# Kernel optimization log

Measured on AMD Instinct MI355X. Metric: run time of the kernel, lower is better.

The kernel has to match this reference:

```python
import jax, jax.numpy as jnp
import numpy as np

B, C, H, W = 4, 256, 64, 64
G, K, PAD, STRIDE, DIL, DWK = 8, 3, 1, 1, 1, 3
P = K * K
GC = C // G


def _dwconv(x, w, b, pad):
    # x: (B,C,H,W), w: (C,1,k,k) depthwise
    y = jax.lax.conv_general_dilated(x, w, (1, 1), [(pad, pad), (pad, pad)],
                                     feature_group_count=C,
                                     dimension_numbers=('NCHW', 'OIHW', 'NCHW'))
    return y + b[None, :, None, None]


def _conv1x1(x, w, b):
    # x: (B,Cin,H,W), w: (Cin,Cout)
    return jnp.einsum('bchw,cd->bdhw', x, w) + b[None, :, None, None]


def _ln(x, g, b, eps=1e-5):
    mu = x.mean(-1, keepdims=True)
    var = ((x - mu) ** 2).mean(-1, keepdims=True)
    return (x - mu) * jax.lax.rsqrt(var + eps) * g + b


def _bilinear_sample(img, grid):
    # img: (GC, Hp, Wp); grid: (L, P, 2) in [-1,1]; F.grid_sample bilinear,
    # padding_mode='zeros', align_corners=False
    gc, Hp, Wp = img.shape
    ix = ((grid[..., 0] + 1.0) * Wp - 1.0) * 0.5
    iy = ((grid[..., 1] + 1.0) * Hp - 1.0) * 0.5
    x0 = jnp.floor(ix); y0 = jnp.floor(iy)
    x1 = x0 + 1.0;      y1 = y0 + 1.0
    imgf = img.reshape(gc, Hp * Wp)

    def gather(yy, xx):
        valid = (xx >= 0) & (xx <= Wp - 1) & (yy >= 0) & (yy <= Hp - 1)
        xi = jnp.clip(xx, 0, Wp - 1).astype(jnp.int32)
        yi = jnp.clip(yy, 0, Hp - 1).astype(jnp.int32)
        return imgf[:, yi * Wp + xi] * valid  # (GC, L, P)

    w00 = (x1 - ix) * (y1 - iy); w01 = (ix - x0) * (y1 - iy)
    w10 = (x1 - ix) * (iy - y0); w11 = (ix - x0) * (iy - y0)
    return (gather(y0, x0) * w00 + gather(y0, x1) * w01 +
            gather(y1, x0) * w10 + gather(y1, x1) * w11)


def _dcnv3_core(x, offset, mask):
    # x: (B,H,W,C); offset: (B,H,W,G*P*2); mask: (B,H,W,G*P) softmaxed over P
    xp = jnp.pad(x, ((0, 0), (PAD, PAD), (PAD, PAD), (0, 0)))
    Hp, Wp = H + 2 * PAD, W + 2 * PAD
    base = (DIL * (K - 1)) // 2 + 0.5
    ref_y = (base + jnp.arange(H, dtype=jnp.float32) * STRIDE) / Hp
    ref_x = (base + jnp.arange(W, dtype=jnp.float32) * STRIDE) / Wp
    ref = jnp.stack([jnp.broadcast_to(ref_x[None, :], (H, W)),
                     jnp.broadcast_to(ref_y[:, None], (H, W))], -1)  # (H,W,2) (x,y)
    lin = jnp.arange(K, dtype=jnp.float32) * DIL - (DIL * (K - 1)) // 2
    gx, gy = jnp.meshgrid(lin, lin, indexing='ij')  # x-outer (torch meshgrid order)
    dil_grid = jnp.stack([gx / Wp, gy / Hp], -1).reshape(P, 2)
    loc = ref[:, :, None, None, :] + dil_grid[None, None, None, :, :]  # (H,W,1,P,2)
    loc = jnp.broadcast_to(loc, (H, W, G, P, 2))[None]
    norm = jnp.array([Wp, Hp], jnp.float32)
    loc = loc + offset.reshape(B, H, W, G, P, 2) / norm  # offset_scale=1.0
    sg = 2.0 * loc - 1.0  # (B,H,W,G,P,2)
    xin = xp.reshape(B, Hp, Wp, G, GC).transpose(0, 3, 4, 1, 2).reshape(B * G, GC, Hp, Wp)
    sgf = sg.reshape(B, H * W, G, P, 2).transpose(0, 2, 1, 3, 4).reshape(B * G, H * W, P, 2)
    sampled = jax.vmap(_bilinear_sample)(xin, sgf)  # (B*G, GC, HW, P)
    m = mask.reshape(B, H * W, G, P).transpose(0, 2, 1, 3).reshape(B * G, 1, H * W, P)
    out = (sampled * m).sum(-1)  # (B*G, GC, HW)
    return out.reshape(B, G, GC, H * W).transpose(0, 3, 1, 2).reshape(B, H, W, C)


def _dcn(x, inproj_w, inproj_b, dw_w, dw_b, ln_g, ln_b,
         off_w, off_b, mask_w, mask_b, outproj_w, outproj_b):
    # x: (B,H,W,C) -> DCNv3_pytorch forward
    xproj = x @ inproj_w + inproj_b
    x1 = _dwconv(x.transpose(0, 3, 1, 2), dw_w, dw_b, (DWK - 1) // 2).transpose(0, 2, 3, 1)
    x1 = jax.nn.gelu(_ln(x1, ln_g, ln_b), approximate=False)
    offset = x1 @ off_w + off_b
    m = jax.nn.softmax((x1 @ mask_w + mask_b).reshape(B, H, W, G, P), -1).reshape(B, H, W, G * P)
    out = _dcnv3_core(xproj, offset, m)
    return out @ outproj_w + outproj_b


def _forward(x, proj1_w, proj1_b, conv0_w, conv0_b, inproj_w, inproj_b,
             dw_w, dw_b, ln_g, ln_b, off_w, off_b, mask_w, mask_b,
             outproj_w, outproj_b, conv_w, conv_b, proj2_w, proj2_b):
    shortcut = x
    h = jax.nn.gelu(_conv1x1(x, proj1_w, proj1_b), approximate=False)
    u = h
    h = _dwconv(h, conv0_w, conv0_b, 2)  # 5x5 depthwise, pad 2
    attn = _dcn(h.transpose(0, 2, 3, 1), inproj_w, inproj_b, dw_w, dw_b,
                ln_g, ln_b, off_w, off_b, mask_w, mask_b, outproj_w, outproj_b)
    attn = _conv1x1(attn.transpose(0, 3, 1, 2), conv_w, conv_b)
    h = _conv1x1(u * attn, proj2_w, proj2_b)
    return h + shortcut


def setup_inputs():
    key = jax.random.key(0)
    ks = jax.random.split(key, 12)
    s = lambda k, shape, fan: jax.random.normal(k, shape, jnp.float32) / np.sqrt(fan)
    return {
        'x': jax.random.normal(ks[0], (B, C, H, W), jnp.float32),
        'proj1_w': s(ks[1], (C, C), C), 'proj1_b': jnp.zeros((C,), jnp.float32),
        'conv0_w': s(ks[2], (C, 1, 5, 5), 25), 'conv0_b': jnp.zeros((C,), jnp.float32),
        'inproj_w': s(ks[3], (C, C), C), 'inproj_b': jnp.zeros((C,), jnp.float32),
        'dw_w': s(ks[4], (C, 1, DWK, DWK), DWK * DWK), 'dw_b': jnp.zeros((C,), jnp.float32),
        'ln_g': jnp.ones((C,), jnp.float32), 'ln_b': jnp.zeros((C,), jnp.float32),
        'off_w': s(ks[5], (C, G * P * 2), C) * 0.1, 'off_b': jnp.zeros((G * P * 2,), jnp.float32),
        'mask_w': s(ks[6], (C, G * P), C), 'mask_b': jnp.zeros((G * P,), jnp.float32),
        'outproj_w': s(ks[7], (C, C), C), 'outproj_b': jnp.zeros((C,), jnp.float32),
        'conv_w': s(ks[8], (C, C), C), 'conv_b': jnp.zeros((C,), jnp.float32),
        'proj2_w': s(ks[9], (C, C), C), 'proj2_b': jnp.zeros((C,), jnp.float32),
    }


def reference(x, proj1_w, proj1_b, conv0_w, conv0_b, inproj_w, inproj_b,
              dw_w, dw_b, ln_g, ln_b, off_w, off_b, mask_w, mask_b,
              outproj_w, outproj_b, conv_w, conv_b, proj2_w, proj2_b):
    return _forward(x, proj1_w, proj1_b, conv0_w, conv0_b, inproj_w, inproj_b,
                    dw_w, dw_b, ln_g, ln_b, off_w, off_b, mask_w, mask_b,
                    outproj_w, outproj_b, conv_w, conv_b, proj2_w, proj2_b)
```

## Files before the change

### kernel.cpp

```cpp
#include <hip/hip_runtime.h>
#include <cstddef>

#define HW    4096
#define NPIX  16384
#define CCH   256

typedef __attribute__((ext_vector_type(8))) short bf16x8;
typedef __attribute__((ext_vector_type(4))) float f32x4;

__device__ __forceinline__ float gelu_f(float x){
    return 0.5f * x * (1.0f + erff(x * 0.70710678118654752f));
}

__device__ __forceinline__ unsigned short bf_rne(float f){
    unsigned u = __float_as_uint(f);
    u += 0x7FFFu + ((u >> 16) & 1u);
    return (unsigned short)(u >> 16);
}

__device__ __forceinline__ void split2(const float4 a, const float4 b, bf16x8& hi, bf16x8& lo){
    const float v[8] = {a.x,a.y,a.z,a.w,b.x,b.y,b.z,b.w};
    #pragma unroll
    for (int j = 0; j < 8; j++){
        const unsigned u = __float_as_uint(v[j]);
        hi[j] = (short)(unsigned short)(u >> 16);
        lo[j] = (short)bf_rne(v[j] - __uint_as_float(u & 0xFFFF0000u));
    }
}

__global__ __launch_bounds__(256) void k_prep(const float* __restrict__ w5,
                                              const float* __restrict__ w3,
                                              float* __restrict__ wT,
                                              float* __restrict__ wT3){
    const int c = threadIdx.x;
    const int j = blockIdx.x;
    wT[j * CCH + c] = w5[c * 25 + j];
    if (j < 9) wT3[j * CCH + c] = w3[c * 9 + j];
}

__global__ __launch_bounds__(256) void k_prep_w(
    const float* __restrict__ w0, const float* __restrict__ w1, const float* __restrict__ w2,
    const float* __restrict__ w3, const float* __restrict__ w4,
    const float* __restrict__ offw, const float* __restrict__ maskw,
    const float* __restrict__ offb, const float* __restrict__ maskb,
    unsigned short* __restrict__ wsp, float* __restrict__ bcat)
{
    __shared__ float tile[64][65];
    const int id = blockIdx.y;
    const int m0 = (blockIdx.x & 3) * 64;
    const int k0 = (blockIdx.x >> 2) * 64;
    const int tx = threadIdx.x & 63, tg = threadIdx.x >> 6;
    unsigned short* hi = wsp + (size_t)id * 131072;
    unsigned short* lo = hi + 65536;

    const int m = m0 + tx;
    const float* src = nullptr; int stride = 0; bool valid = true;
    if (id == 5){
        if (m < 144){ src = offw + m; stride = 144; }
        else if (m < 216){ src = maskw + (m - 144); stride = 72; }
        else valid = false;
    } else {
        const float* s = (id==0)?w0:(id==1)?w1:(id==2)?w2:(id==3)?w3:w4;
        src = s + m; stride = 256;
    }
    #pragma unroll
    for (int i = 0; i < 16; i++){
        const int kl = tg * 16 + i;
        tile[kl][tx] = valid ? src[(size_t)(k0 + kl) * stride] : 0.f;
    }
    __syncthreads();
    #pragma unroll
    for (int i = 0; i < 16; i++){
        const int ml = tg * 16 + i;
        const float f = tile[tx][ml];
        const unsigned u = __float_as_uint(f);
        const size_t o = (size_t)(m0 + ml) * 256 + k0 + tx;
        hi[o] = (unsigned short)(u >> 16);
        lo[o] = bf_rne(f - __uint_as_float(u & 0xFFFF0000u));
    }
    if (id == 5 && blockIdx.x == 0){
        const int t = threadIdx.x;
        if (t < 216) bcat[t] = (t < 144) ? offb[t] : maskb[t - 144];
        else if (t < 224) bcat[t] = 0.f;
    }
}

__global__ __launch_bounds__(256) void k_transpose(const float* __restrict__ in,
                                                   float* __restrict__ out){
    __shared__ float tile[64][65];
    const int b = blockIdx.z, c0 = blockIdx.y * 64, hw0 = blockIdx.x * 64;
    const int tx = threadIdx.x & 63, tg = threadIdx.x >> 6;
    #pragma unroll
    for (int i = 0; i < 16; i++){
        const int c_l = tg * 16 + i;
        tile[c_l][tx] = in[(size_t)(b * CCH + c0 + c_l) * HW + hw0 + tx];
    }
    __syncthreads();
    #pragma unroll
    for (int i = 0; i < 16; i++){
        const int hw_l = tg * 16 + i;
        out[(size_t)(b * HW + hw0 + hw_l) * CCH + c0 + tx] = tile[tx][hw_l];
    }
}

template<int EPI, bool MUL>
__global__ __launch_bounds__(256) void k_gemm_bf(
    const float* __restrict__ A, const float* __restrict__ A2,
    const unsigned short* __restrict__ Whi, const unsigned short* __restrict__ Wlo,
    const float* __restrict__ bias, const float* __restrict__ resid,
    float* __restrict__ out, const int M, const int ldc)
{
    const int rows0 = blockIdx.x * 64;
    const int cols0 = blockIdx.y * 128;
    const int lane = threadIdx.x & 63;
    const int w    = threadIdx.x >> 6;
    const int wm = (w >> 1) * 32, wn = (w & 1) * 64;
    const int lr = lane & 15;
    const int kg = lane >> 4;
    const int kl = kg * 8;

    const float* A0 = A + (size_t)(rows0 + wm + lr) * 256 + kl;
    const float* A1 = A0 + 16 * 256;
    const float* M0 = MUL ? (A2 + (size_t)(rows0 + wm + lr) * 256 + kl) : nullptr;
    const float* M1 = MUL ? (M0 + 16 * 256) : nullptr;
    const int c0 = cols0 + wn + lr;
    const unsigned short* Wh = Whi + (size_t)c0 * 256 + kl;
    const unsigned short* Wl = Wlo + (size_t)c0 * 256 + kl;

    const f32x4 z = {0.f, 0.f, 0.f, 0.f};
    f32x4 acc[2][4] = {{z,z,z,z},{z,z,z,z}};

    #pragma unroll 2
    for (int kt = 0; kt < 8; kt++){
        const int k0 = kt * 32;
        float4 a0 = *reinterpret_cast<const float4*>(A0 + k0);
        float4 a1 = *reinterpret_cast<const float4*>(A0 + k0 + 4);
        float4 a2 = *reinterpret_cast<const float4*>(A1 + k0);
        float4 a3 = *reinterpret_cast<const float4*>(A1 + k0 + 4);
        if (MUL){
            const float4 u0 = *reinterpret_cast<const float4*>(M0 + k0);
            const float4 u1 = *reinterpret_cast<const float4*>(M0 + k0 + 4);
            const float4 u2 = *reinterpret_cast<const float4*>(M1 + k0);
            const float4 u3 = *reinterpret_cast<const float4*>(M1 + k0 + 4);
            a0.x*=u0.x; a0.y*=u0.y; a0.z*=u0.z; a0.w*=u0.w;
            a1.x*=u1.x; a1.y*=u1.y; a1.z*=u1.z; a1.w*=u1.w;
            a2.x*=u2.x; a2.y*=u2.y; a2.z*=u2.z; a2.w*=u2.w;
            a3.x*=u3.x; a3.y*=u3.y; a3.z*=u3.z; a3.w*=u3.w;
        }
        bf16x8 ah0, al0, ah1, al1;
        split2(a0, a1, ah0, al0);
        split2(a2, a3, ah1, al1);
        #pragma unroll
        for (int nf = 0; nf < 4; nf++){
            const size_t wo = (size_t)(nf * 16) * 256 + k0;
            const bf16x8 bh = *reinterpret_cast<const bf16x8*>(Wh + wo);
            const bf16x8 bl = *reinterpret_cast<const bf16x8*>(Wl + wo);
            acc[0][nf] = __builtin_amdgcn_mfma_f32_16x16x32_bf16(ah0, bh, acc[0][nf], 0, 0, 0);
            acc[0][nf] = __builtin_amdgcn_mfma_f32_16x16x32_bf16(ah0, bl, acc[0][nf], 0, 0, 0);
            acc[0][nf] = __builtin_amdgcn_mfma_f32_16x16x32_bf16(al0, bh, acc[0][nf], 0, 0, 0);
            acc[1][nf] = __builtin_amdgcn_mfma_f32_16x16x32_bf16(ah1, bh, acc[1][nf], 0, 0, 0);
            acc[1][nf] = __builtin_amdgcn_mfma_f32_16x16x32_bf16(ah1, bl, acc[1][nf], 0, 0, 0);
            acc[1][nf] = __builtin_amdgcn_mfma_f32_16x16x32_bf16(al1, bh, acc[1][nf], 0, 0, 0);
        }
    }

    const int r4 = kg * 4;
    if (EPI == 2){
        #pragma unroll
        for (int nf = 0; nf < 4; nf++){
            const int col = c0 + nf * 16;
            const float bs = bias[col];
            #pragma unroll
            for (int mf = 0; mf < 2; mf++){
                const int row = rows0 + wm + mf * 16 + r4;
                const int bimg = row >> 12;
                const int hw = row & (HW - 1);
                const size_t addr = ((size_t)(bimg * CCH + col)) * HW + hw;
                const float4 rv = *reinterpret_cast<const float4*>(resid + addr);
                float4 o;
                o.x = acc[mf][nf][0] + bs + rv.x;
                o.y = acc[mf][nf][1] + bs + rv.y;
                o.z = acc[mf][nf][2] + bs + rv.z;
                o.w = acc[mf][nf][3] + bs + rv.w;
                *reinterpret_cast<float4*>(out + addr) = o;
            }
        }
    } else {
        #pragma unroll
        for (int nf = 0; nf < 4; nf++){
            const int col = c0 + nf * 16;
            if (col < M){
                const float bs = bias[col];
                #pragma unroll
                for (int mf = 0; mf < 2; mf++){
                    const int rowb = rows0 + wm + mf * 16 + r4;
                    #pragma unroll
                    for (int r = 0; r < 4; r++){
                        float v = acc[mf][nf][r] + bs;
                        if (EPI == 1) v = gelu_f(v);
                        out[(size_t)(rowb + r) * ldc + col] = v;
                    }
                }
            }
        }
    }
}

__global__ __launch_bounds__(256) void k_dwconv5(const float* __restrict__ in,
                                                 const float* __restrict__ wT,
                                                 const float* __restrict__ bias,
                                                 float* __restrict__ out){
    const int lane = threadIdx.x & 63;
    const int pq   = threadIdx.x >> 6;
    const int n = blockIdx.x * 4 + pq;
    const int x = n & 63, y = (n >> 6) & 63, b = n >> 12;
    const int c = lane * 4;
    const float* bp = in + (size_t)(b * HW) * CCH + c;
    float4 acc = *reinterpret_cast<const float4*>(bias + c);
    #pragma unroll
    for (int k = 0; k < 25; k++){
        const int dy = k / 5 - 2, dx = k % 5 - 2;
        const int yy = y + dy, xx = x + dx;
        const float m = (((unsigned)yy < 64u) & ((unsigned)xx < 64u)) ? 1.f : 0.f;
        const int yc = min(max(yy, 0), 63), xc = min(max(xx, 0), 63);
        const float4 iv = *reinterpret_cast<const float4*>(bp + (size_t)(yc * 64 + xc) * CCH);
        const float4 wv = *reinterpret_cast<const float4*>(wT + k * CCH + c);
        acc.x = fmaf(iv.x, wv.x * m, acc.x);
        acc.y = fmaf(iv.y, wv.y * m, acc.y);
        acc.z = fmaf(iv.z, wv.z * m, acc.z);
        acc.w = fmaf(iv.w, wv.w * m, acc.w);
    }
    *reinterpret_cast<float4*>(out + (size_t)n * CCH + c) = acc;
}

__global__ __launch_bounds__(256) void k_dw3_ln_gelu(const float* __restrict__ in,
                                                     const float* __restrict__ wT3,
                                                     const float* __restrict__ b3,
                                                     const float* __restrict__ g,
                                                     const float* __restrict__ bta,
                                                     float* __restrict__ out){
    const int lane = threadIdx.x & 63;
    const int pq   = threadIdx.x >> 6;
    const int n = blockIdx.x * 4 + pq;
    const int x = n & 63, y = (n >> 6) & 63, b = n >> 12;
    const int c = lane * 4;
    const float* bp = in + (size_t)(b * HW) * CCH + c;
    float4 acc = *reinterpret_cast<const float4*>(b3 + c);
    #pragma unroll
    for (int k = 0; k < 9; k++){
        const int dy = k / 3 - 1, dx = k % 3 - 1;
        const int yy = y + dy, xx = x + dx;
        const float m = (((unsigned)yy < 64u) & ((unsigned)xx < 64u)) ? 1.f : 0.f;
        const int yc = min(max(yy, 0), 63), xc = min(max(xx, 0), 63);
        const float4 iv = *reinterpret_cast<const float4*>(bp + (size_t)(yc * 64 + xc) * CCH);
        const float4 wv = *reinterpret_cast<const float4*>(wT3 + k * CCH + c);
        acc.x = fmaf(iv.x, wv.x * m, acc.x);
        acc.y = fmaf(iv.y, wv.y * m, acc.y);
        acc.z = fmaf(iv.z, wv.z * m, acc.z);
        acc.w = fmaf(iv.w, wv.w * m, acc.w);
    }
    float s  = acc.x + acc.y + acc.z + acc.w;
    float s2 = acc.x*acc.x + acc.y*acc.y + acc.z*acc.z + acc.w*acc.w;
    #pragma unroll
    for (int o = 32; o > 0; o >>= 1){
        s  += __shfl_xor(s, o);
        s2 += __shfl_xor(s2, o);
    }
    const float mu  = s  * (1.f / 256.f);
    const float var = s2 * (1.f / 256.f) - mu * mu;
    const float r   = rsqrtf(var + 1e-5f);
    const float4 gv = *reinterpret_cast<const float4*>(g + c);
    const float4 bv = *reinterpret_cast<const float4*>(bta + c);
    float4 o;
    o.x = gelu_f((acc.x - mu) * r * gv.x + bv.x);
    o.y = gelu_f((acc.y - mu) * r * gv.y + bv.y);
    o.z = gelu_f((acc.z - mu) * r * gv.z + bv.z);
    o.w = gelu_f((acc.w - mu) * r * gv.w + bv.w);
    *reinterpret_cast<float4*>(out + (size_t)n * CCH + c) = o;
}

__global__ __launch_bounds__(256) void k_dcn(const float* __restrict__ xproj,
                                             const float* __restrict__ om,
                                             float* __restrict__ out){
    const int lane = threadIdx.x & 63;
    const int pq   = threadIdx.x >> 6;
    const int n = blockIdx.x * 4 + pq;
    const int gI = lane >> 3, cq = lane & 7;
    const int x = n & 63, y = (n >> 6) & 63, b = n >> 12;
    const float* off = om + (size_t)n * 216 + gI * 18;
    const float* lg  = om + (size_t)n * 216 + 144 + gI * 9;
    float l[9]; float mx = -1e30f;
    #pragma unroll
    for (int p = 0; p < 9; p++){ l[p] = lg[p]; mx = fmaxf(mx, l[p]); }
    float ssum = 0.f;
    #pragma unroll
    for (int p = 0; p < 9; p++){ l[p] = expf(l[p] - mx); ssum += l[p]; }
    const float inv = 1.f / ssum;
    const float* base = xproj + (size_t)b * HW * CCH + gI * 32 + cq * 4;
    float4 acc = {0.f, 0.f, 0.f, 0.f};
    #pragma unroll
    for (int p = 0; p < 9; p++){
        const float2 o2 = *reinterpret_cast<const float2*>(off + p * 2);
        const float ix = (float)(x + p / 3) + o2.x;
        const float iy = (float)(y + p % 3) + o2.y;
        const float x0f = floorf(ix), y0f = floorf(iy);
        const float wx1 = ix - x0f, wy1 = iy - y0f;
        const float wx0 = 1.f - wx1, wy0 = 1.f - wy1;
        const int ux = (int)x0f - 1, uy = (int)y0f - 1;
        const bool X0 = (unsigned)ux     < 64u, X1 = (unsigned)(ux+1) < 64u;
        const bool Y0 = (unsigned)uy     < 64u, Y1 = (unsigned)(uy+1) < 64u;
        const int ux0 = min(max(ux,     0), 63), ux1 = min(max(ux + 1, 0), 63);
        const int uy0 = min(max(uy,     0), 63), uy1 = min(max(uy + 1, 0), 63);
        const float mp = l[p] * inv;
        const float w00 = wx0 * wy0 * ((X0 & Y0) ? mp : 0.f);
        const float w01 = wx1 * wy0 * ((X1 & Y0) ? mp : 0.f);
        const float w10 = wx0 * wy1 * ((X0 & Y1) ? mp : 0.f);
        const float w11 = wx1 * wy1 * ((X1 & Y1) ? mp : 0.f);
        const float4 v00 = *reinterpret_cast<const float4*>(base + (size_t)(uy0 * 64 + ux0) * CCH);
        const float4 v01 = *reinterpret_cast<const float4*>(base + (size_t)(uy0 * 64 + ux1) * CCH);
        const float4 v10 = *reinterpret_cast<const float4*>(base + (size_t)(uy1 * 64 + ux0) * CCH);
        const float4 v11 = *reinterpret_cast<const float4*>(base + (size_t)(uy1 * 64 + ux1) * CCH);
        acc.x = fmaf(w00, v00.x, fmaf(w01, v01.x, fmaf(w10, v10.x, fmaf(w11, v11.x, acc.x))));
        acc.y = fmaf(w00, v00.y, fmaf(w01, v01.y, fmaf(w10, v10.y, fmaf(w11, v11.y, acc.y))));
        acc.z = fmaf(w00, v00.z, fmaf(w01, v01.z, fmaf(w10, v10.z, fmaf(w11, v11.z, acc.z))));
        acc.w = fmaf(w00, v00.w, fmaf(w01, v01.w, fmaf(w10, v10.w, fmaf(w11, v11.w, acc.w))));
    }
    *reinterpret_cast<float4*>(out + (size_t)n * CCH + gI * 32 + cq * 4) = acc;
}

extern "C" void kernel_launch(void* const* d_in, const int* in_sizes, int n_in,
                              void* d_out, int out_size, void* d_ws, size_t ws_size,
                              hipStream_t stream){
    const float* x         = (const float*)d_in[0];
    const float* proj1_w   = (const float*)d_in[1];
    const float* proj1_b   = (const float*)d_in[2];
    const float* conv0_w   = (const float*)d_in[3];
    const float* conv0_b   = (const float*)d_in[4];
    const float* inproj_w  = (const float*)d_in[5];
    const float* inproj_b  = (const float*)d_in[6];
    const float* dw_w      = (const float*)d_in[7];
    const float* dw_b      = (const float*)d_in[8];
    const float* ln_g      = (const float*)d_in[9];
    const float* ln_b      = (const float*)d_in[10];
    const float* off_w     = (const float*)d_in[11];
    const float* off_b     = (const float*)d_in[12];
    const float* mask_w    = (const float*)d_in[13];
    const float* mask_b    = (const float*)d_in[14];
    const float* outproj_w = (const float*)d_in[15];
    const float* outproj_b = (const float*)d_in[16];
    const float* conv_w    = (const float*)d_in[17];
    const float* conv_b    = (const float*)d_in[18];
    const float* proj2_w   = (const float*)d_in[19];
    const float* proj2_b   = (const float*)d_in[20];
    float* outp = (float*)d_out;

    const size_t NC = (size_t)NPIX * CCH;
    float* b0 = (float*)d_ws;
    float* b1 = b0 + NC;
    float* b2 = b1 + NC;
    float* b3 = outp;
    unsigned short* wsp = (unsigned short*)(b2 + NC);
    float* bcat = (float*)(wsp + 6 * 131072);
    float* wT   = b3;
    float* wT3  = b3 + 25 * CCH;

    const unsigned short* whi[6]; const unsigned short* wlo[6];
    for (int i = 0; i < 6; i++){ whi[i] = wsp + (size_t)i * 131072; wlo[i] = whi[i] + 65536; }

    const dim3 G(256, 2);

    k_prep<<<25,256,0,stream>>>(conv0_w, dw_w, wT, wT3);
    k_prep_w<<<dim3(16,6),256,0,stream>>>(proj1_w, inproj_w, outproj_w, conv_w, proj2_w,
                                          off_w, mask_w, off_b, mask_b, wsp, bcat);
    k_transpose<<<dim3(64,4,4),256,0,stream>>>(x, b0);
    k_gemm_bf<1,false><<<G,256,0,stream>>>(b0, nullptr, whi[0], wlo[0], proj1_b, nullptr, b1, 256, 256);
    k_dwconv5<<<4096,256,0,stream>>>(b1, wT, conv0_b, b2);
    k_dw3_ln_gelu<<<4096,256,0,stream>>>(b2, wT3, dw_b, ln_g, ln_b, b0);
    k_gemm_bf<0,false><<<G,256,0,stream>>>(b2, nullptr, whi[1], wlo[1], inproj_b, nullptr, b3, 256, 256);
    k_gemm_bf<0,false><<<G,256,0,stream>>>(b0, nullptr, whi[5], wlo[5], bcat, nullptr, b2, 216, 216);
    k_dcn<<<4096,256,0,stream>>>(b3, b2, b0);
    k_gemm_bf<0,false><<<G,256,0,stream>>>(b0, nullptr, whi[2], wlo[2], outproj_b, nullptr, b3, 256, 256);
    k_gemm_bf<0,false><<<G,256,0,stream>>>(b3, nullptr, whi[3], wlo[3], conv_b, nullptr, b2, 256, 256);
    k_gemm_bf<2,true><<<G,256,0,stream>>>(b1, b2, whi[4], wlo[4], proj2_b, x, outp, 256, 256);
}
```

Measured before the change: 359.2 us.

## Fold outproj and conv weights into one GEMM and widen GEMM tiles to full N

After: 391.5 us. 9.0% more time.

```diff
diff --git a/kernel.cpp b/kernel.cpp
--- a/kernel.cpp
+++ b/kernel.cpp
@@ -18,13 +18,14 @@
     return (unsigned short)(u >> 16);
 }
 
-__device__ __forceinline__ void split2(const float4 a, const float4 b, bf16x8& hi, bf16x8& lo){
+__device__ __forceinline__ void split_cheap(const float4 a, const float4 b, bf16x8& hi, bf16x8& lo){
     const float v[8] = {a.x,a.y,a.z,a.w,b.x,b.y,b.z,b.w};
     #pragma unroll
     for (int j = 0; j < 8; j++){
         const unsigned u = __float_as_uint(v[j]);
         hi[j] = (short)(unsigned short)(u >> 16);
-        lo[j] = (short)bf_rne(v[j] - __uint_as_float(u & 0xFFFF0000u));
+        const float r = v[j] - __uint_as_float(u & 0xFFFF0000u);
+        lo[j] = (short)(unsigned short)(__float_as_uint(r) >> 16);
     }
 }
 
@@ -38,9 +39,31 @@
     if (j < 9) wT3[j * CCH + c] = w3[c * 9 + j];
 }
 
+__global__ __launch_bounds__(256) void k_compose(const float* __restrict__ ow,
+                                                 const float* __restrict__ cw,
+                                                 const float* __restrict__ ob,
+                                                 const float* __restrict__ cb,
+                                                 float* __restrict__ woc,
+                                                 float* __restrict__ boc){
+    const int m = threadIdx.x;
+    if (blockIdx.x == 256){
+        float acc = cb[m];
+        #pragma unroll 4
+        for (int k = 0; k < 256; k++) acc = fmaf(ob[k], cw[k * 256 + m], acc);
+        boc[m] = acc;
+    } else {
+        const int r = blockIdx.x;
+        const float* orow = ow + r * 256;
+        float acc = 0.f;
+        #pragma unroll 4
+        for (int k = 0; k < 256; k++) acc = fmaf(orow[k], cw[k * 256 + m], acc);
+        woc[r * 256 + m] = acc;
+    }
+}
+
 __global__ __launch_bounds__(256) void k_prep_w(
     const float* __restrict__ w0, const float* __restrict__ w1, const float* __restrict__ w2,
-    const float* __restrict__ w3, const float* __restrict__ w4,
+    const float* __restrict__ w3,
     const float* __restrict__ offw, const float* __restrict__ maskw,
     const float* __restrict__ offb, const float* __restrict__ maskb,
     unsigned short* __restrict__ wsp, float* __restrict__ bcat)
@@ -55,12 +78,12 @@
 
     const int m = m0 + tx;
     const float* src = nullptr; int stride = 0; bool valid = true;
-    if (id == 5){
+    if (id == 4){
         if (m < 144){ src = offw + m; stride = 144; }
         else if (m < 216){ src = maskw + (m - 144); stride = 72; }
         else valid = false;
     } else {
-        const float* s = (id==0)?w0:(id==1)?w1:(id==2)?w2:(id==3)?w3:w4;
+        const float* s = (id==0)?w0:(id==1)?w1:(id==2)?w2:w3;
         src = s + m; stride = 256;
     }
     #pragma unroll
@@ -78,7 +101,7 @@
         hi[o] = (unsigned short)(u >> 16);
         lo[o] = bf_rne(f - __uint_as_float(u & 0xFFFF0000u));
     }
-    if (id == 5 && blockIdx.x == 0){
+    if (id == 4 && blockIdx.x == 0){
         const int t = threadIdx.x;
         if (t < 216) bcat[t] = (t < 144) ? offb[t] : maskb[t - 144];
         else if (t < 224) bcat[t] = 0.f;
@@ -110,96 +133,77 @@
     const float* __restrict__ bias, const float* __restrict__ resid,
     float* __restrict__ out, const int M, const int ldc)
 {
-    const int rows0 = blockIdx.x * 64;
-    const int cols0 = blockIdx.y * 128;
+    const int rows0 = blockIdx.x * 32;
     const int lane = threadIdx.x & 63;
     const int w    = threadIdx.x >> 6;
-    const int wm = (w >> 1) * 32, wn = (w & 1) * 64;
+    const int wm = (w >> 1) * 16;
+    const int wn = (w & 1) * 128;
     const int lr = lane & 15;
     const int kg = lane >> 4;
     const int kl = kg * 8;
 
-    const float* A0 = A + (size_t)(rows0 + wm + lr) * 256 + kl;
-    const float* A1 = A0 + 16 * 256;
-    const float* M0 = MUL ? (A2 + (size_t)(rows0 + wm + lr) * 256 + kl) : nullptr;
-    const float* M1 = MUL ? (M0 + 16 * 256) : nullptr;
-    const int c0 = cols0 + wn + lr;
+    const float* Ap = A + (size_t)(rows0 + wm + lr) * 256 + kl;
+    const float* Mp = MUL ? (A2 + (size_t)(rows0 + wm + lr) * 256 + kl) : nullptr;
+    const int c0 = wn + lr;
     const unsigned short* Wh = Whi + (size_t)c0 * 256 + kl;
     const unsigned short* Wl = Wlo + (size_t)c0 * 256 + kl;
 
     const f32x4 z = {0.f, 0.f, 0.f, 0.f};
-    f32x4 acc[2][4] = {{z,z,z,z},{z,z,z,z}};
+    f32x4 acc[8] = {z,z,z,z,z,z,z,z};
 
     #pragma unroll 2
     for (int kt = 0; kt < 8; kt++){
         const int k0 = kt * 32;
-        float4 a0 = *reinterpret_cast<const float4*>(A0 + k0);
-        float4 a1 = *reinterpret_cast<const float4*>(A0 + k0 + 4);
-        float4 a2 = *reinterpret_cast<const float4*>(A1 + k0);
-        float4 a3 = *reinterpret_cast<const float4*>(A1 + k0 + 4);
+        float4 a0 = *reinterpret_cast<const float4*>(Ap + k0);
+        float4 a1 = *reinterpret_cast<const float4*>(Ap + k0 + 4);
         if (MUL){
-            const float4 u0 = *reinterpret_cast<const float4*>(M0 + k0);
-            const float4 u1 = *reinterpret_cast<const float4*>(M0 + k0 + 4);
-            const float4 u2 = *reinterpret_cast<const float4*>(M1 + k0);
-            const float4 u3 = *reinterpret_cast<const float4*>(M1 + k0 + 4);
+            const float4 u0 = *reinterpret_cast<const float4*>(Mp + k0);
+            const float4 u1 = *reinterpret_cast<const float4*>(Mp + k0 + 4);
             a0.x*=u0.x; a0.y*=u0.y; a0.z*=u0.z; a0.w*=u0.w;
             a1.x*=u1.x; a1.y*=u1.y; a1.z*=u1.z; a1.w*=u1.w;
-            a2.x*=u2.x; a2.y*=u2.y; a2.z*=u2.z; a2.w*=u2.w;
-            a3.x*=u3.x; a3.y*=u3.y; a3.z*=u3.z; a3.w*=u3.w;
         }
-        bf16x8 ah0, al0, ah1, al1;
-        split2(a0, a1, ah0, al0);
-        split2(a2, a3, ah1, al1);
+        bf16x8 ah, al;
+        split_cheap(a0, a1, ah, al);
         #pragma unroll
-        for (int nf = 0; nf < 4; nf++){
+        for (int nf = 0; nf < 8; nf++){
             const size_t wo = (size_t)(nf * 16) * 256 + k0;
             const bf16x8 bh = *reinterpret_cast<const bf16x8*>(Wh + wo);
             const bf16x8 bl = *reinterpret_cast<const bf16x8*>(Wl + wo);
-            acc[0][nf] = __builtin_amdgcn_mfma_f32_16x16x32_bf16(ah0, bh, acc[0][nf], 0, 0, 0);
-            acc[0][nf] = __builtin_amdgcn_mfma_f32_16x16x32_bf16(ah0, bl, acc[0][nf], 0, 0, 0);
-            acc[0][nf] = __builtin_amdgcn_mfma_f32_16x16x32_bf16(al0, bh, acc[0][nf], 0, 0, 0);
-            acc[1][nf] = __builtin_amdgcn_mfma_f32_16x16x32_bf16(ah1, bh, acc[1][nf], 0, 0, 0);
-            acc[1][nf] = __builtin_amdgcn_mfma_f32_16x16x32_bf16(ah1, bl, acc[1][nf], 0, 0, 0);
-            acc[1][nf] = __builtin_amdgcn_mfma_f32_16x16x32_bf16(al1, bh, acc[1][nf], 0, 0, 0);
+            acc[nf] = __builtin_amdgcn_mfma_f32_16x16x32_bf16(ah, bh, acc[nf], 0, 0, 0);
+            acc[nf] = __builtin_amdgcn_mfma_f32_16x16x32_bf16(ah, bl, acc[nf], 0, 0, 0);
+            acc[nf] = __builtin_amdgcn_mfma_f32_16x16x32_bf16(al, bh, acc[nf], 0, 0, 0);
         }
     }
 
     const int r4 = kg * 4;
+    const int rowb = rows0 + wm + r4;
     if (EPI == 2){
+        const int bimg = rowb >> 12;
+        const int hw   = rowb & (HW - 1);
         #pragma unroll
-        for (int nf = 0; nf < 4; nf++){
+        for (int nf = 0; nf < 8; nf++){
             const int col = c0 + nf * 16;
             const float bs = bias[col];
-            #pragma unroll
-            for (int mf = 0; mf < 2; mf++){
-                const int row = rows0 + wm + mf * 16 + r4;
-                const int bimg = row >> 12;
-                const int hw = row & (HW - 1);
-                const size_t addr = ((size_t)(bimg * CCH + col)) * HW + hw;
-                const float4 rv = *reinterpret_cast<const float4*>(resid + addr);
-                float4 o;
-                o.x = acc[mf][nf][0] + bs + rv.x;
-                o.y = acc[mf][nf][1] + bs + rv.y;
-                o.z = acc[mf][nf][2] + bs + rv.z;
-                o.w = acc[mf][nf][3] + bs + rv.w;
-                *reinterpret_cast<float4*>(out + addr) = o;
-            }
+            const size_t addr = ((size_t)(bimg * CCH + col)) * HW + hw;
+            const float4 rv = *reinterpret_cast<const float4*>(resid + addr);
+            float4 o;
+            o.x = acc[nf][0] + bs + rv.x;
+            o.y = acc[nf][1] + bs + rv.y;
+            o.z = acc[nf][2] + bs + rv.z;
+            o.w = acc[nf][3] + bs + rv.w;
+            *reinterpret_cast<float4*>(out + addr) = o;
         }
     } else {
         #pragma unroll
-        for (int nf = 0; nf < 4; nf++){
+        for (int nf = 0; nf < 8; nf++){
             const int col = c0 + nf * 16;
             if (col < M){
                 const float bs = bias[col];
                 #pragma unroll
-                for (int mf = 0; mf < 2; mf++){
-                    const int rowb = rows0 + wm + mf * 16 + r4;
-                    #pragma unroll
-                    for (int r = 0; r < 4; r++){
-                        float v = acc[mf][nf][r] + bs;
-                        if (EPI == 1) v = gelu_f(v);
-                        out[(size_t)(rowb + r) * ldc + col] = v;
-                    }
+                for (int r = 0; r < 4; r++){
+                    float v = acc[nf][r] + bs;
+                    if (EPI == 1) v = gelu_f(v);
+                    out[(size_t)(rowb + r) * ldc + col] = v;
                 }
             }
         }
@@ -360,26 +364,26 @@
     float* b2 = b1 + NC;
     float* b3 = outp;
     unsigned short* wsp = (unsigned short*)(b2 + NC);
-    float* bcat = (float*)(wsp + 6 * 131072);
+    float* bcat = (float*)(wsp + 5 * 131072);
+    float* woc  = bcat + 224;
+    float* boc  = woc + 65536;
     float* wT   = b3;
     float* wT3  = b3 + 25 * CCH;
 
-    const unsigned short* whi[6]; const unsigned short* wlo[6];
-    for (int i = 0; i < 6; i++){ whi[i] = wsp + (size_t)i * 131072; wlo[i] = whi[i] + 65536; }
-
-    const dim3 G(256, 2);
+    const unsigned short* whi[5]; const unsigned short* wlo[5];
+    for (int i = 0; i < 5; i++){ whi[i] = wsp + (size_t)i * 131072; wlo[i] = whi[i] + 65536; }
 
     k_prep<<<25,256,0,stream>>>(conv0_w, dw_w, wT, wT3);
-    k_prep_w<<<dim3(16,6),256,0,stream>>>(proj1_w, inproj_w, outproj_w, conv_w, proj2_w,
+    k_compose<<<257,256,0,stream>>>(outproj_w, conv_w, outproj_b, conv_b, woc, boc);
+    k_prep_w<<<dim3(16,5),256,0,stream>>>(proj1_w, inproj_w, woc, proj2_w,
                                           off_w, mask_w, off_b, mask_b, wsp, bcat);
     k_transpose<<<dim3(64,4,4),256,0,stream>>>(x, b0);
-    k_gemm_bf<1,false><<<G,256,0,stream>>>(b0, nullptr, whi[0], wlo[0], proj1_b, nullptr, b1, 256, 256);
+    k_gemm_bf<1,false><<<512,256,0,stream>>>(b0, nullptr, whi[0], wlo[0], proj1_b, nullptr, b1, 256, 256);
     k_dwconv5<<<4096,256,0,stream>>>(b1, wT, conv0_b, b2);
     k_dw3_ln_gelu<<<4096,256,0,stream>>>(b2, wT3, dw_b, ln_g, ln_b, b0);
-    k_gemm_bf<0,false><<<G,256,0,stream>>>(b2, nullptr, whi[1], wlo[1], inproj_b, nullptr, b3, 256, 256);
-    k_gemm_bf<0,false><<<G,256,0,stream>>>(b0, nullptr, whi[5], wlo[5], bcat, nullptr, b2, 216, 216);
+    k_gemm_bf<0,false><<<512,256,0,stream>>>(b2, nullptr, whi[1], wlo[1], inproj_b, nullptr, b3, 256, 256);
+    k_gemm_bf<0,false><<<512,256,0,stream>>>(b0, nullptr, whi[4], wlo[4], bcat, nullptr, b2, 216, 216);
     k_dcn<<<4096,256,0,stream>>>(b3, b2, b0);
-    k_gemm_bf<0,false><<<G,256,0,stream>>>(b0, nullptr, whi[2], wlo[2], outproj_b, nullptr, b3, 256, 256);
-    k_gemm_bf<0,false><<<G,256,0,stream>>>(b3, nullptr, whi[3], wlo[3], conv_b, nullptr, b2, 256, 256);
-    k_gemm_bf<2,true><<<G,256,0,stream>>>(b1, b2, whi[4], wlo[4], proj2_b, x, outp, 256, 256);
-}
+    k_gemm_bf<0,false><<<512,256,0,stream>>>(b0, nullptr, whi[2], wlo[2], boc, nullptr, b2, 256, 256);
+    k_gemm_bf<2,true><<<512,256,0,stream>>>(b1, b2, whi[3], wlo[3], proj2_b, x, outp, 256, 256);
+}
```
